# Optimization experiments

Measured on AMD Instinct MI355X. Metric: run time of the kernel, lower is better.

The kernel has to match this reference:

```python
import jax, jax.numpy as jnp
import numpy as np
import math

# Model dims (see shape_source)
BATCH, SEQ, HH, WW = 32, 128, 32, 32   # x: (B, seq_len, H, W); L = H*W = 1024
D_MODEL = 1024                          # hidden_dim
N2 = 4                                  # n=8 -> 4 complex S4D modes
L_MAX = 64                              # SSM kernel length (l_max)


def _layernorm(x, gamma, beta, eps=1e-5):
    mu = jnp.mean(x, axis=-1, keepdims=True)
    var = jnp.var(x, axis=-1, keepdims=True)
    return (x - mu) * jax.lax.rsqrt(var + eps) * gamma + beta


def setup_inputs() -> dict:
    key = jax.random.key(0)
    ks = jax.random.split(key, 12)
    d_in = SEQ  # d_input = d_output = seq_len
    inp = {
        "x": jax.random.normal(ks[0], (BATCH, SEQ, HH, WW), dtype=jnp.float32),
        # encoder Linear(d_input -> d_model)
        "W_enc": jax.random.normal(ks[1], (d_in, D_MODEL), dtype=jnp.float32) / math.sqrt(d_in),
        "b_enc": jnp.zeros((D_MODEL,), dtype=jnp.float32),
        # S4D SSM parameters (per d_model channel, N2 complex modes)
        "log_dt": (jax.random.uniform(ks[2], (D_MODEL,), dtype=jnp.float32)
                   * (math.log(0.1) - math.log(0.001)) + math.log(0.001)),
        "A_log_real": jnp.full((D_MODEL, N2), math.log(0.5), dtype=jnp.float32),
        "A_imag": jnp.broadcast_to(math.pi * jnp.arange(N2, dtype=jnp.float32), (D_MODEL, N2)).copy(),
        "C_real": jax.random.normal(ks[3], (D_MODEL, N2), dtype=jnp.float32) * 0.5,
        "C_imag": jax.random.normal(ks[4], (D_MODEL, N2), dtype=jnp.float32) * 0.5,
        "D": jax.random.normal(ks[5], (D_MODEL,), dtype=jnp.float32),
        # position-wise GLU mixing Linear(d_model -> 2*d_model)
        "W_glu": jax.random.normal(ks[6], (D_MODEL, 2 * D_MODEL), dtype=jnp.float32) / math.sqrt(D_MODEL),
        "b_glu": jnp.zeros((2 * D_MODEL,), dtype=jnp.float32),
        "ln_gamma": jnp.ones((D_MODEL,), dtype=jnp.float32),
        "ln_beta": jnp.zeros((D_MODEL,), dtype=jnp.float32),
        # decoder Linear(d_model -> d_output)
        "W_dec": jax.random.normal(ks[7], (D_MODEL, d_in), dtype=jnp.float32) / math.sqrt(D_MODEL),
        "b_dec": jnp.zeros((d_in,), dtype=jnp.float32),
    }
    return inp


def reference(x, W_enc, b_enc, log_dt, A_log_real, A_imag, C_real, C_imag, D,
              W_glu, b_glu, ln_gamma, ln_beta, W_dec, b_dec):
    Bsz, S, Hh, Ww = x.shape
    L = Hh * Ww
    u = x.reshape(Bsz, S, L)                                  # (B, d_input, L)
    # encoder applied per position along L
    h = jnp.einsum('bdl,de->ble', u, W_enc) + b_enc           # (B, L, d_model)

    # ---- S4D kernel (ZOH discretization, B=1, diagonal A) ----
    dt = jnp.exp(log_dt)                                      # (d,)
    A = -jnp.exp(A_log_real) + 1j * A_imag                    # (d, n2) complex
    Cc = C_real + 1j * C_imag
    dtA = A * dt[:, None]                                     # (d, n2)
    Bd = (jnp.exp(dtA) - 1.0) / A                             # ZOH input matrix
    t = jnp.arange(L_MAX)
    vand = jnp.exp(dtA[:, :, None] * t)                       # (d, n2, l_max)
    K = 2.0 * jnp.einsum('dn,dnl->dl', Cc * Bd, vand).real    # (d, l_max)

    # ---- causal FFT convolution along L + skip D*u ----
    z = jnp.swapaxes(h, 1, 2)                                 # (B, d, L)
    n_fft = L + L_MAX
    y = jnp.fft.irfft(jnp.fft.rfft(z, n=n_fft) * jnp.fft.rfft(K, n=n_fft), n=n_fft)[..., :L]
    y = y + D[:, None] * z                                    # (B, d, L)

    # ---- block: GELU -> GLU mixing -> residual -> LayerNorm ----
    y = jax.nn.gelu(jnp.swapaxes(y, 1, 2))                    # (B, L, d)
    g = y @ W_glu + b_glu                                     # (B, L, 2d)
    g = g[..., :D_MODEL] * jax.nn.sigmoid(g[..., D_MODEL:])
    h = _layernorm(h + g, ln_gamma, ln_beta)                  # (B, L, d)

    out = h @ W_dec + b_dec                                   # (B, L, d_output)
    out = jnp.swapaxes(out, 1, 2).reshape(Bsz, S, Hh, Ww)
    return out
```

## Files before the change

### kernel.cpp

```cpp
#include <hip/hip_runtime.h>
#include <hip/hip_bf16.h>
#include <math.h>

#define B_ 32
#define S_ 128
#define L_ 1024
#define D_ 1024

typedef unsigned short u16;
typedef __attribute__((ext_vector_type(8))) __bf16 bf16x8;
typedef __attribute__((ext_vector_type(8))) short short8;
typedef __attribute__((ext_vector_type(4))) float f32x4;

__device__ __forceinline__ float bf2f(u16 u) {
    return __uint_as_float(((unsigned)u) << 16);
}
__device__ __forceinline__ u16 f2bf(float f) {
    unsigned u = __float_as_uint(f);
    u += 0x7FFF + ((u >> 16) & 1);
    return (u16)(u >> 16);
}
__device__ __forceinline__ float gelu_tanh(float x) {
    float x3 = x * x * x;
    float t = tanhf(0.7978845608028654f * (x + 0.044715f * x3));
    return 0.5f * x * (1.0f + t);
}
__device__ __forceinline__ float sigmoidf(float x) {
    return 1.0f / (1.0f + expf(-x));
}
__device__ __forceinline__ void gld16(const void* g, void* l) {
    __builtin_amdgcn_global_load_lds((const __attribute__((address_space(1))) void*)g,
                                     (__attribute__((address_space(3))) void*)l, 16, 0, 0);
}

__device__ __forceinline__ void tcast_body(
        const float* __restrict__ src, u16* __restrict__ dst, int R, int C,
        const float* __restrict__ rowscale, int bx, int by, int t,
        float (*tile)[65]) {
    int c0 = bx * 64, r0 = by * 64;
    #pragma unroll
    for (int p = 0; p < 4; ++p) {
        int fid = p * 256 + t;
        int rr = fid >> 4, cc = (fid & 15) * 4;
        float4 v = *(const float4*)&src[(size_t)(r0 + rr) * C + c0 + cc];
        float sc = rowscale ? rowscale[r0 + rr] : 1.0f;
        tile[rr][cc + 0] = v.x * sc; tile[rr][cc + 1] = v.y * sc;
        tile[rr][cc + 2] = v.z * sc; tile[rr][cc + 3] = v.w * sc;
    }
    __syncthreads();
    #pragma unroll
    for (int p = 0; p < 4; ++p) {
        int fid = p * 256 + t;
        int rr = fid >> 4, cc = (fid & 15) * 4;
        ushort4 o;
        o.x = f2bf(tile[cc + 0][rr]);
        o.y = f2bf(tile[cc + 1][rr]);
        o.z = f2bf(tile[cc + 2][rr]);
        o.w = f2bf(tile[cc + 3][rr]);
        *(ushort4*)&dst[(size_t)(c0 + rr) * R + r0 + cc] = o;
    }
}

__global__ __launch_bounds__(256) void k_prep(
        const float* __restrict__ Wg, u16* __restrict__ WgT,
        const float* __restrict__ Wd, const float* __restrict__ gam,
        u16* __restrict__ WdT,
        const float* __restrict__ We, u16* __restrict__ WeT,
        const float* __restrict__ x, u16* __restrict__ xb,
        const float* __restrict__ ldt, const float* __restrict__ Alr,
        const float* __restrict__ Aim, const float* __restrict__ Cr,
        const float* __restrict__ Ci, float* __restrict__ Kt,
        const float* __restrict__ bet, const float* __restrict__ bd,
        float* __restrict__ c12) {
    __shared__ float tile[64][65];
    __shared__ float r1[4], r2[4];
    int blk = blockIdx.x;
    int t = threadIdx.x;
    if (blk < 512) {
        tcast_body(Wg, WgT, 1024, 2048, nullptr, blk & 31, blk >> 5, t, tile);
    } else if (blk < 544) {
        int id = blk - 512;
        tcast_body(Wd, WdT, 1024, 128, gam, id & 1, id >> 1, t, tile);
    } else if (blk < 576) {
        int id = blk - 544;
        tcast_body(We, WeT, 128, 1024, nullptr, id & 15, id >> 4, t, tile);
    } else if (blk < 1600) {
        int id = blk - 576;
        int bz = id >> 5;
        tcast_body(x + (size_t)bz * 131072, xb + (size_t)bz * 131072,
                   128, 1024, nullptr, id & 15, (id >> 4) & 1, t, tile);
    } else if (blk < 1856) {
        int tid = (blk - 1600) * 256 + t;
        int d = tid & (D_ - 1);
        int j = tid >> 10;
        float dt = expf(ldt[d]);
        float acc = 0.f;
        #pragma unroll
        for (int n = 0; n < 4; ++n) {
            float ar = -expf(Alr[d * 4 + n]);
            float ai = Aim[d * 4 + n];
            float wr = ar * dt, wi = ai * dt;
            float ew = expf(wr);
            float sw, cw; sincosf(wi, &sw, &cw);
            float ur = ew * cw - 1.0f, ui = ew * sw;
            float inv = 1.0f / (ar * ar + ai * ai);
            float bdr = (ur * ar + ui * ai) * inv;
            float bdi = (ui * ar - ur * ai) * inv;
            float cr = Cr[d * 4 + n], ci = Ci[d * 4 + n];
            float cbr = cr * bdr - ci * bdi;
            float cbi = cr * bdi + ci * bdr;
            float ej = expf(wr * (float)j);
            float sj, cj; sincosf(wi * (float)j, &sj, &cj);
            acc += 2.0f * ej * (cbr * cj - cbi * sj);
        }
        Kt[j * D_ + d] = acc;
    } else {
        int s = blk - 1856;
        float a1 = 0.f, a2 = 0.f;
        #pragma unroll
        for (int it = 0; it < 4; ++it) {
            int k = it * 256 + t;
            float w = Wd[(size_t)k * 128 + s];
            a1 += gam[k] * w;
            a2 += bet[k] * w;
        }
        #pragma unroll
        for (int off = 32; off > 0; off >>= 1) {
            a1 += __shfl_down(a1, off);
            a2 += __shfl_down(a2, off);
        }
        int wid = t >> 6, lane = t & 63;
        if (lane == 0) { r1[wid] = a1; r2[wid] = a2; }
        __syncthreads();
        if (t == 0) {
            c12[s] = r1[0] + r1[1] + r1[2] + r1[3];
            c12[128 + s] = r2[0] + r2[1] + r2[2] + r2[3] + bd[s];
        }
    }
}

__global__ __launch_bounds__(256, 4) void k_enc_mfma(
        const u16* __restrict__ xb, const u16* __restrict__ WeT,
        const float* __restrict__ be, u16* __restrict__ hb) {
    __shared__ __align__(16) u16 S[17408];
    u16* As = S;
    u16* Bs = S + 8192;
    int t = threadIdx.x;
    int lane = t & 63, wid = t >> 6;
    int wr = wid & 1, wc = wid >> 1;
    int orig = blockIdx.x;
    int wgid = (orig & 7) * 256 + (orig >> 3);
    int m0 = (wgid >> 3) * 128;
    int e0 = (wgid & 7) * 128;

    int gofs = (((lane & 7) ^ ((lane >> 3) & 7)) * 8);
    int rloc[4];
    #pragma unroll
    for (int c = 0; c < 4; ++c) rloc[c] = (wid * 4 + c) * 8 + (lane >> 3);
    int co[2];
    co[0] = (((lane >> 4) + 0) ^ (lane & 7)) * 8;
    co[1] = (((lane >> 4) + 4) ^ (lane & 7)) * 8;
    int arow[4], brow[4];
    #pragma unroll
    for (int i = 0; i < 4; ++i) arow[i] = (wr * 64 + i * 16 + (lane & 15)) * 64;
    #pragma unroll
    for (int q = 0; q < 4; ++q) brow[q] = (wc * 64 + q * 16 + (lane & 15)) * 64;

    f32x4 acc[4][4] = {};
    #pragma unroll
    for (int kt = 0; kt < 2; ++kt) {
        if (kt) __syncthreads();
        int k0 = kt * 64;
        #pragma unroll
        for (int c = 0; c < 4; ++c) {
            int ch = wid * 4 + c;
            gld16(&xb[(size_t)(m0 + rloc[c]) * 128 + k0 + gofs], &As[ch * 512]);
            gld16(&WeT[(size_t)(e0 + rloc[c]) * 128 + k0 + gofs], &Bs[ch * 512]);
        }
        __syncthreads();
        #pragma unroll
        for (int kh = 0; kh < 2; ++kh) {
            bf16x8 af[4], bfr[4];
            #pragma unroll
            for (int i = 0; i < 4; ++i) af[i] = *(const bf16x8*)&As[arow[i] + co[kh]];
            #pragma unroll
            for (int q = 0; q < 4; ++q) bfr[q] = *(const bf16x8*)&Bs[brow[q] + co[kh]];
            __builtin_amdgcn_s_setprio(1);
            #pragma unroll
            for (int i = 0; i < 4; ++i)
                #pragma unroll
                for (int q = 0; q < 4; ++q)
                    acc[i][q] = __builtin_amdgcn_mfma_f32_16x16x32_bf16(af[i], bfr[q], acc[i][q], 0, 0, 0);
            __builtin_amdgcn_s_setprio(0);
        }
    }
    __syncthreads();
    #pragma unroll
    for (int q = 0; q < 4; ++q) {
        int e = wc * 64 + q * 16 + (lane & 15);
        float bias = be[e0 + e];
        #pragma unroll
        for (int i = 0; i < 4; ++i)
            #pragma unroll
            for (int r = 0; r < 4; ++r) {
                int m = wr * 64 + i * 16 + (lane >> 4) * 4 + r;
                S[m * 136 + e] = f2bf(acc[i][q][r] + bias);
            }
    }
    __syncthreads();
    #pragma unroll
    for (int p = 0; p < 8; ++p) {
        int fid = p * 256 + t;
        int row = fid >> 4, cg = (fid & 15) * 8;
        *(uint4*)&hb[(size_t)(m0 + row) * 1024 + e0 + cg] = *(const uint4*)&S[row * 136 + cg];
    }
}

__global__ __launch_bounds__(256) void k_conv(
        const u16* __restrict__ hb, const float* __restrict__ Kt,
        const float* __restrict__ Dv, u16* __restrict__ yg) {
    __shared__ float hs[128][68];
    int b = blockIdx.y;
    int d0 = blockIdx.x * 64;
    int t = threadIdx.x;
    int dl = t & 63, lg = t >> 6;
    {
        int r = 64 + (t >> 2), cg0 = (t & 3) * 16;
        #pragma unroll
        for (int j = 0; j < 4; ++j)
            *(float4*)&hs[r][cg0 + j * 4] = make_float4(0.f, 0.f, 0.f, 0.f);
    }
    float kr[64];
    #pragma unroll
    for (int j = 0; j < 64; ++j) kr[j] = Kt[j * 1024 + d0 + dl];
    float Dd = Dv[d0 + dl];
    int lr = t >> 2, cg = (t & 3) * 16;
    uint4 pref0, pref1;
#define LOADP(IT) { const u16* src = &hb[((size_t)b * 1024 + (IT) * 64 + lr) * 1024 + d0 + cg]; \
    pref0 = *(const uint4*)&src[0]; pref1 = *(const uint4*)&src[8]; }
    LOADP(0);
    for (int it = 0; it < 16; ++it) {
        int l0 = it * 64;
        {
            int row = (l0 + lr) & 127;
            const u16* pu0 = (const u16*)&pref0;
            const u16* pu1 = (const u16*)&pref1;
            #pragma unroll
            for (int e = 0; e < 8; ++e) hs[row][cg + e] = bf2f(pu0[e]);
            #pragma unroll
            for (int e = 0; e < 8; ++e) hs[row][cg + 8 + e] = bf2f(pu1[e]);
        }
        __syncthreads();
        if (it < 15) LOADP(it + 1);
        float acc[16] = {};
        int rb = l0 + 65 + lg * 16;
        #pragma unroll
        for (int s = 0; s < 15; ++s) {
            float hv = hs[(rb + s) & 127][dl];
            #pragma unroll
            for (int i = 0; i <= 14; ++i)
                if (i <= s) acc[i] = fmaf(kr[i + 63 - s], hv, acc[i]);
        }
        #pragma unroll
        for (int s = 15; s < 64; ++s) {
            float hv = hs[(rb + s) & 127][dl];
            #pragma unroll
            for (int i = 0; i < 16; ++i)
                acc[i] = fmaf(kr[i + 63 - s], hv, acc[i]);
        }
        #pragma unroll
        for (int s = 64; s < 79; ++s) {
            float hv = hs[(rb + s) & 127][dl];
            #pragma unroll
            for (int i = 1; i < 16; ++i)
                if (i >= s - 63) acc[i] = fmaf(kr[i + 63 - s], hv, acc[i]);
        }
        #pragma unroll
        for (int i = 0; i < 16; ++i) {
            int l = l0 + lg * 16 + i;
            float z = hs[l & 127][dl];
            float y = acc[i] + Dd * z;
            yg[((size_t)b * 1024 + l) * 1024 + d0 + dl] = f2bf(gelu_tanh(y));
        }
        __syncthreads();
    }
#undef LOADP
}

__global__ __launch_bounds__(512, 2) void k_glu256(
        const u16* __restrict__ yg, const u16* __restrict__ WgT,
        const float* __restrict__ bg, u16* __restrict__ hb) {
    __shared__ u16 S[65536];
    int t = threadIdx.x;
    int lane = t & 63, wid = t >> 6;
    int wr = wid >> 2, wc = wid & 3;

    int orig = blockIdx.x;
    int wgid = (orig & 7) * 128 + (orig >> 3);
    int m0 = (wgid >> 3) * 256;
    int p0g = (wgid & 7) * 128;

    int gofs = (((lane & 7) ^ ((lane >> 3) & 7)) * 8);
    int ch0 = wid * 2, ch1 = ch0 + 1;
    int dst0 = ch0 * 512 + lane * 8;
    int dst1 = ch1 * 512 + lane * 8;
    int gmA[2][2], gmB[2][2];
    #pragma unroll
    for (int h = 0; h < 2; ++h) {
        #pragma unroll
        for (int j = 0; j < 2; ++j) {
            int ch = ch0 + j;
            gmA[h][j] = m0 + (ch >> 3) * 128 + h * 64 + (ch & 7) * 8 + (lane >> 3);
            int r = (ch >> 2) * 64 + h * 32 + (ch & 3) * 8 + (lane >> 3);
            gmB[h][j] = ((r >> 4) & 1) * 1024 + p0g + (((r >> 5) << 4) | (r & 15));
        }
    }
    int co[2];
    co[0] = (((lane >> 4) + 0) ^ (lane & 7)) * 8;
    co[1] = (((lane >> 4) + 4) ^ (lane & 7)) * 8;
    int arow[4], brow[2];
    #pragma unroll
    for (int i = 0; i < 4; ++i) arow[i] = (wr * 64 + i * 16 + (lane & 15)) * 64;
    #pragma unroll
    for (int q = 0; q < 2; ++q) brow[q] = (wc * 32 + q * 16 + (lane & 15)) * 64;

#define GLD_A(H, BUF, K0) { u16* d_ = &S[((BUF) * 2 + (H)) * 8192]; \
    gld16(&yg[(size_t)gmA[H][0] * 1024 + (K0) + gofs], d_ + dst0); \
    gld16(&yg[(size_t)gmA[H][1] * 1024 + (K0) + gofs], d_ + dst1); }
#define GLD_B(H, BUF, K0) { u16* d_ = &S[32768 + ((BUF) * 2 + (H)) * 8192]; \
    gld16(&WgT[(size_t)gmB[H][0] * 1024 + (K0) + gofs], d_ + dst0); \
    gld16(&WgT[(size_t)gmB[H][1] * 1024 + (K0) + gofs], d_ + dst1); }

#define RD_AH(MS) { const u16* Ar_ = &S[(cbuf * 2 + (MS)) * 8192]; \
    _Pragma("unroll") for (int i = 0; i < 4; ++i) { \
        a_[i][0] = *(const bf16x8*)&Ar_[arow[i] + co[0]]; \
        a_[i][1] = *(const bf16x8*)&Ar_[arow[i] + co[1]]; } }
#define RD_BH(NS, BB) { const u16* Br_ = &S[32768 + (cbuf * 2 + (NS)) * 8192]; \
    _Pragma("unroll") for (int q = 0; q < 2; ++q) { \
        BB[q][0] = *(const bf16x8*)&Br_[brow[q] + co[0]]; \
        BB[q][1] = *(const bf16x8*)&Br_[brow[q] + co[1]]; } }
#define MFMA16(MS, NS, BB) { __builtin_amdgcn_s_setprio(1); \
    _Pragma("unroll") for (int i = 0; i < 4; ++i) \
        _Pragma("unroll") for (int q = 0; q < 2; ++q) { \
            acc[(MS) * 4 + i][(NS) * 2 + q] = __builtin_amdgcn_mfma_f32_16x16x32_bf16( \
                a_[i][0], BB[q][0], acc[(MS) * 4 + i][(NS) * 2 + q], 0, 0, 0); \
            acc[(MS) * 4 + i][(NS) * 2 + q] = __builtin_amdgcn_mfma_f32_16x16x32_bf16( \
                a_[i][1], BB[q][1], acc[(MS) * 4 + i][(NS) * 2 + q], 0, 0, 0); } \
    __builtin_amdgcn_s_setprio(0); }

    f32x4 acc[8][4] = {};
    bf16x8 a_[4][2], b0_[2][2], b1_[2][2];

    GLD_A(0, 0, 0); GLD_B(0, 0, 0); GLD_B(1, 0, 0); GLD_A(1, 0, 0);
    GLD_A(0, 1, 64); GLD_B(0, 1, 64);

    for (int kt = 0; kt < 15; ++kt) {
        int cbuf = kt & 1, nbuf = cbuf ^ 1;
        int k1 = (kt + 1) * 64, k2 = (kt + 2) * 64;
        asm volatile("s_waitcnt vmcnt(4)" ::: "memory");
        __builtin_amdgcn_s_barrier();
        __builtin_amdgcn_sched_barrier(0);
        RD_AH(0); RD_BH(0, b0_); RD_BH(1, b1_);
        GLD_B(1, nbuf, k1);
        GLD_A(1, nbuf, k1);
        MFMA16(0, 0, b0_);
        MFMA16(0, 1, b1_);
        RD_AH(1);
        __builtin_amdgcn_s_barrier();
        __builtin_amdgcn_sched_barrier(0);
        if (kt < 14) { GLD_A(0, cbuf, k2); GLD_B(0, cbuf, k2); }
        MFMA16(1, 0, b0_);
        MFMA16(1, 1, b1_);
    }
    {
        int cbuf = 1;
        asm volatile("s_waitcnt vmcnt(0)" ::: "memory");
        __builtin_amdgcn_s_barrier();
        __builtin_amdgcn_sched_barrier(0);
        RD_AH(0); RD_BH(0, b0_); RD_BH(1, b1_);
        MFMA16(0, 0, b0_);
        MFMA16(0, 1, b1_);
        RD_AH(1);
        MFMA16(1, 0, b0_);
        MFMA16(1, 1, b1_);
    }
#undef GLD_A
#undef GLD_B
#undef RD_AH
#undef RD_BH
#undef MFMA16

    #pragma unroll
    for (int i = 0; i < 8; ++i) {
        #pragma unroll
        for (int pb = 0; pb < 2; ++pb) {
            int col = p0g + (wc * 2 + pb) * 16 + (lane & 15);
            float b1v = bg[col];
            float b2v = bg[1024 + col];
            #pragma unroll
            for (int r = 0; r < 4; ++r) {
                int m = m0 + wr * 128 + i * 16 + (lane >> 4) * 4 + r;
                size_t idx = (size_t)m * 1024 + col;
                float g1 = acc[i][pb * 2][r] + b1v;
                float g2 = acc[i][pb * 2 + 1][r] + b2v;
                hb[idx] = f2bf(bf2f(hb[idx]) + g1 * sigmoidf(g2));
            }
        }
    }
}

__global__ __launch_bounds__(256) void k_dec_mfma(
        const u16* __restrict__ hb, const u16* __restrict__ WdT,
        const float* __restrict__ c12, float* __restrict__ out) {
    __shared__ __align__(16) char smem[66560];
    u16* As = (u16*)smem;
    u16* Bs = (u16*)(smem + 32768);
    float* Ts = (float*)smem;
    float* muL = (float*)(smem + 65536);
    float* rsL = (float*)(smem + 65536 + 512);
    int t = threadIdx.x;
    int lane = t & 63, wid = t >> 6;
    int wr = wid & 1, wc = wid >> 1;
    int m0 = blockIdx.x * 128;
    int bb = m0 >> 10, l0 = m0 & 1023;

    int gsrc = (((lane & 7) ^ (lane >> 3)) * 8);
    int rr4[4];
    #pragma unroll
    for (int c = 0; c < 4; ++c) rr4[c] = (wid * 4 + c) * 8 + (lane >> 3);
    int co[2];
    co[0] = (((lane >> 4) + 0) ^ (lane & 7)) * 8;
    co[1] = (((lane >> 4) + 4) ^ (lane & 7)) * 8;
    int arow[4], brow[4];
    #pragma unroll
    for (int i = 0; i < 4; ++i) arow[i] = (wr * 64 + i * 16 + (lane & 15)) * 64;
    #pragma unroll
    for (int q = 0; q < 4; ++q) brow[q] = (wc * 64 + q * 16 + (lane & 15)) * 64;

    f32x4 acc[4][4] = {};
    float s1[4] = {}, s2[4] = {};
    #pragma unroll
    for (int c = 0; c < 4; ++c) {
        int ch = wid * 4 + c;
        gld16(&hb[(size_t)(m0 + rr4[c]) * 1024 + gsrc], &As[0 * 8192 + ch * 512]);
        gld16(&WdT[(size_t)rr4[c] * 1024 + gsrc], &Bs[0 * 8192 + ch * 512]);
    }
    __syncthreads();
    int cur = 0;
    for (int kt = 0; kt < 16; ++kt) {
        if (kt < 15) {
            int k0 = (kt + 1) * 64;
            #pragma unroll
            for (int c = 0; c < 4; ++c) {
                int ch = wid * 4 + c;
                gld16(&hb[(size_t)(m0 + rr4[c]) * 1024 + k0 + gsrc], &As[(cur ^ 1) * 8192 + ch * 512]);
                gld16(&WdT[(size_t)rr4[c] * 1024 + k0 + gsrc], &Bs[(cur ^ 1) * 8192 + ch * 512]);
            }
        }
        #pragma unroll
        for (int kh = 0; kh < 2; ++kh) {
            bf16x8 af[4], bfr[4];
            #pragma unroll
            for (int i = 0; i < 4; ++i) af[i] = *(const bf16x8*)&As[cur * 8192 + arow[i] + co[kh]];
            #pragma unroll
            for (int q = 0; q < 4; ++q) bfr[q] = *(const bf16x8*)&Bs[cur * 8192 + brow[q] + co[kh]];
            if (wid < 2) {
                #pragma unroll
                for (int i = 0; i < 4; ++i) {
                    short8 sa = *(short8*)&af[i];
                    #pragma unroll
                    for (int e = 0; e < 8; ++e) {
                        float v = bf2f((u16)sa[e]);
                        s1[i] += v;
                        s2[i] = fmaf(v, v, s2[i]);
                    }
                }
            }
            __builtin_amdgcn_s_setprio(1);
            #pragma unroll
            for (int i = 0; i < 4; ++i)
                #pragma unroll
                for (int q = 0; q < 4; ++q)
                    acc[i][q] = __builtin_amdgcn_mfma_f32_16x16x32_bf16(af[i], bfr[q], acc[i][q], 0, 0, 0);
            __builtin_amdgcn_s_setprio(0);
        }
        __syncthreads();
        cur ^= 1;
    }
    if (wid < 2) {
        #pragma unroll
        for (int i = 0; i < 4; ++i) {
            s1[i] += __shfl_xor(s1[i], 16);
            s2[i] += __shfl_xor(s2[i], 16);
            s1[i] += __shfl_xor(s1[i], 32);
            s2[i] += __shfl_xor(s2[i], 32);
            if (lane < 16) {
                int ml = wr * 64 + i * 16 + lane;
                float mu = s1[i] * (1.0f / 1024.0f);
                float var = s2[i] * (1.0f / 1024.0f) - mu * mu;
                muL[ml] = mu;
                rsL[ml] = rsqrtf(var + 1e-5f);
            }
        }
    }
    __syncthreads();
    #pragma unroll
    for (int ro = 0; ro < 2; ++ro) {
        if (wc == ro) {
            #pragma unroll
            for (int i = 0; i < 4; ++i)
                #pragma unroll
                for (int q = 0; q < 4; ++q) {
                    int sl = q * 16 + (lane & 15);
                    float c1v = c12[ro * 64 + sl];
                    float c2v = c12[128 + ro * 64 + sl];
                    #pragma unroll
                    for (int r = 0; r < 4; ++r) {
                        int ml = wr * 64 + i * 16 + (lane >> 4) * 4 + r;
                        float rst = rsL[ml];
                        Ts[sl * 132 + ml] = rst * acc[i][q][r] - muL[ml] * rst * c1v + c2v;
                    }
                }
        }
        __syncthreads();
        #pragma unroll
        for (int p = 0; p < 8; ++p) {
            int fid = p * 256 + t;
            int sl = fid >> 5, c = (fid & 31) * 4;
            float4 v = *(const float4*)&Ts[sl * 132 + c];
            *(float4*)&out[(size_t)bb * 131072 + (size_t)(ro * 64 + sl) * 1024 + l0 + c] = v;
        }
        __syncthreads();
    }
}

extern "C" void kernel_launch(void* const* d_in, const int* in_sizes, int n_in,
                              void* d_out, int out_size, void* d_ws, size_t ws_size,
                              hipStream_t stream) {
    (void)in_sizes; (void)n_in; (void)out_size; (void)ws_size;
    const float* x   = (const float*)d_in[0];
    const float* We  = (const float*)d_in[1];
    const float* be  = (const float*)d_in[2];
    const float* ldt = (const float*)d_in[3];
    const float* Alr = (const float*)d_in[4];
    const float* Aim = (const float*)d_in[5];
    const float* Cr  = (const float*)d_in[6];
    const float* Ci  = (const float*)d_in[7];
    const float* Dv  = (const float*)d_in[8];
    const float* Wg  = (const float*)d_in[9];
    const float* bg  = (const float*)d_in[10];
    const float* gam = (const float*)d_in[11];
    const float* bet = (const float*)d_in[12];
    const float* Wd  = (const float*)d_in[13];
    const float* bd  = (const float*)d_in[14];
    float* out = (float*)d_out;

    u16* hb = (u16*)d_ws;
    u16* yg = hb + 33554432ull;
    float* Kt = (float*)(yg + 33554432ull);
    u16* WgT = (u16*)(Kt + 65536);
    u16* WdT = WgT + 2097152ull;
    u16* WeT = WdT + 131072ull;
    float* c12 = (float*)(WeT + 131072ull);
    u16* xb  = yg;

    k_prep<<<1984, 256, 0, stream>>>(Wg, WgT, Wd, gam, WdT, We, WeT, x, xb,
                                     ldt, Alr, Aim, Cr, Ci, Kt, bet, bd, c12);
    k_enc_mfma<<<2048, 256, 0, stream>>>(xb, WeT, be, hb);
    k_conv<<<dim3(16, 32), 256, 0, stream>>>(hb, Kt, Dv, yg);
    k_glu256<<<1024, 512, 0, stream>>>(yg, WgT, bg, hb);
    k_dec_mfma<<<256, 256, 0, stream>>>(hb, WdT, c12, out);
}
```

Before: 323.9 us.

## Load GLU weight fragments directly from global into registers, skipping LDS staging

The B operand (GLU weights) of the GLU GEMM is now read straight from global memory into per-wave register fragments, with double buffering in even and odd register sets, instead of being staged through shared memory. Only the A tiles still go through LDS, which halves the LDS footprint and removes the B-side LDS reads. The cost is more VGPRs for the prefetched B fragments, a different vmcnt accounting, and uncoalesced 16-byte global reads of the weights that rely on L2 reuse across workgroups.

```diff
diff --git a/kernel.cpp b/kernel.cpp
--- a/kernel.cpp
+++ b/kernel.cpp
@@ -290,7 +290,7 @@
 __global__ __launch_bounds__(512, 2) void k_glu256(
         const u16* __restrict__ yg, const u16* __restrict__ WgT,
         const float* __restrict__ bg, u16* __restrict__ hb) {
-    __shared__ u16 S[65536];
+    __shared__ u16 S[32768];
     int t = threadIdx.x;
     int lane = t & 63, wid = t >> 6;
     int wr = wid >> 2, wc = wid & 3;
@@ -304,91 +304,87 @@
     int ch0 = wid * 2, ch1 = ch0 + 1;
     int dst0 = ch0 * 512 + lane * 8;
     int dst1 = ch1 * 512 + lane * 8;
-    int gmA[2][2], gmB[2][2];
+    int gmA[2][2];
     #pragma unroll
     for (int h = 0; h < 2; ++h) {
         #pragma unroll
         for (int j = 0; j < 2; ++j) {
             int ch = ch0 + j;
             gmA[h][j] = m0 + (ch >> 3) * 128 + h * 64 + (ch & 7) * 8 + (lane >> 3);
-            int r = (ch >> 2) * 64 + h * 32 + (ch & 3) * 8 + (lane >> 3);
-            gmB[h][j] = ((r >> 4) & 1) * 1024 + p0g + (((r >> 5) << 4) | (r & 15));
         }
     }
     int co[2];
     co[0] = (((lane >> 4) + 0) ^ (lane & 7)) * 8;
     co[1] = (((lane >> 4) + 4) ^ (lane & 7)) * 8;
-    int arow[4], brow[2];
+    int arow[4];
     #pragma unroll
     for (int i = 0; i < 4; ++i) arow[i] = (wr * 64 + i * 16 + (lane & 15)) * 64;
-    #pragma unroll
-    for (int q = 0; q < 2; ++q) brow[q] = (wc * 32 + q * 16 + (lane & 15)) * 64;
+    int grB[2][2];
+    #pragma unroll
+    for (int h = 0; h < 2; ++h)
+        #pragma unroll
+        for (int q = 0; q < 2; ++q) {
+            int tr = wc * 64 + h * 32 + q * 16 + (lane & 15);
+            grB[h][q] = ((tr >> 4) & 1) * 1024 + p0g + ((tr >> 5) << 4) + (tr & 15);
+        }
+    int kb[2];
+    kb[0] = (lane >> 4) * 8;
+    kb[1] = ((lane >> 4) + 4) * 8;
 
 #define GLD_A(H, BUF, K0) { u16* d_ = &S[((BUF) * 2 + (H)) * 8192]; \
     gld16(&yg[(size_t)gmA[H][0] * 1024 + (K0) + gofs], d_ + dst0); \
     gld16(&yg[(size_t)gmA[H][1] * 1024 + (K0) + gofs], d_ + dst1); }
-#define GLD_B(H, BUF, K0) { u16* d_ = &S[32768 + ((BUF) * 2 + (H)) * 8192]; \
-    gld16(&WgT[(size_t)gmB[H][0] * 1024 + (K0) + gofs], d_ + dst0); \
-    gld16(&WgT[(size_t)gmB[H][1] * 1024 + (K0) + gofs], d_ + dst1); }
-
-#define RD_AH(MS) { const u16* Ar_ = &S[(cbuf * 2 + (MS)) * 8192]; \
+#define LD_B(BB, K0) { _Pragma("unroll") for (int h = 0; h < 2; ++h) \
+    _Pragma("unroll") for (int q = 0; q < 2; ++q) \
+        _Pragma("unroll") for (int kh = 0; kh < 2; ++kh) \
+            BB[h][q][kh] = *(const bf16x8*)&WgT[(size_t)grB[h][q] * 1024 + (K0) + kb[kh]]; }
+#define RD_AH(MS, CB) { const u16* Ar_ = &S[((CB) * 2 + (MS)) * 8192]; \
     _Pragma("unroll") for (int i = 0; i < 4; ++i) { \
         a_[i][0] = *(const bf16x8*)&Ar_[arow[i] + co[0]]; \
         a_[i][1] = *(const bf16x8*)&Ar_[arow[i] + co[1]]; } }
-#define RD_BH(NS, BB) { const u16* Br_ = &S[32768 + (cbuf * 2 + (NS)) * 8192]; \
-    _Pragma("unroll") for (int q = 0; q < 2; ++q) { \
-        BB[q][0] = *(const bf16x8*)&Br_[brow[q] + co[0]]; \
-        BB[q][1] = *(const bf16x8*)&Br_[brow[q] + co[1]]; } }
 #define MFMA16(MS, NS, BB) { __builtin_amdgcn_s_setprio(1); \
     _Pragma("unroll") for (int i = 0; i < 4; ++i) \
         _Pragma("unroll") for (int q = 0; q < 2; ++q) { \
             acc[(MS) * 4 + i][(NS) * 2 + q] = __builtin_amdgcn_mfma_f32_16x16x32_bf16( \
-                a_[i][0], BB[q][0], acc[(MS) * 4 + i][(NS) * 2 + q], 0, 0, 0); \
+                a_[i][0], BB[(NS)][q][0], acc[(MS) * 4 + i][(NS) * 2 + q], 0, 0, 0); \
             acc[(MS) * 4 + i][(NS) * 2 + q] = __builtin_amdgcn_mfma_f32_16x16x32_bf16( \
-                a_[i][1], BB[q][1], acc[(MS) * 4 + i][(NS) * 2 + q], 0, 0, 0); } \
+                a_[i][1], BB[(NS)][q][1], acc[(MS) * 4 + i][(NS) * 2 + q], 0, 0, 0); } \
     __builtin_amdgcn_s_setprio(0); }
+#define TILE(KT, BB, WAITN, DO_STAGE) { \
+    asm volatile("s_waitcnt vmcnt(" #WAITN ")" ::: "memory"); \
+    __builtin_amdgcn_s_barrier(); \
+    __builtin_amdgcn_sched_barrier(0); \
+    int cb_ = (KT) & 1; \
+    RD_AH(0, cb_); \
+    MFMA16(0, 0, BB); \
+    MFMA16(0, 1, BB); \
+    RD_AH(1, cb_); \
+    __builtin_amdgcn_s_barrier(); \
+    __builtin_amdgcn_sched_barrier(0); \
+    if (DO_STAGE) { GLD_A(0, cb_, ((KT) + 2) * 64); GLD_A(1, cb_, ((KT) + 2) * 64); } \
+    MFMA16(1, 0, BB); \
+    MFMA16(1, 1, BB); \
+    if (DO_STAGE) LD_B(BB, ((KT) + 2) * 64); }
 
     f32x4 acc[8][4] = {};
-    bf16x8 a_[4][2], b0_[2][2], b1_[2][2];
-
-    GLD_A(0, 0, 0); GLD_B(0, 0, 0); GLD_B(1, 0, 0); GLD_A(1, 0, 0);
-    GLD_A(0, 1, 64); GLD_B(0, 1, 64);
-
-    for (int kt = 0; kt < 15; ++kt) {
-        int cbuf = kt & 1, nbuf = cbuf ^ 1;
-        int k1 = (kt + 1) * 64, k2 = (kt + 2) * 64;
-        asm volatile("s_waitcnt vmcnt(4)" ::: "memory");
-        __builtin_amdgcn_s_barrier();
-        __builtin_amdgcn_sched_barrier(0);
-        RD_AH(0); RD_BH(0, b0_); RD_BH(1, b1_);
-        GLD_B(1, nbuf, k1);
-        GLD_A(1, nbuf, k1);
-        MFMA16(0, 0, b0_);
-        MFMA16(0, 1, b1_);
-        RD_AH(1);
-        __builtin_amdgcn_s_barrier();
-        __builtin_amdgcn_sched_barrier(0);
-        if (kt < 14) { GLD_A(0, cbuf, k2); GLD_B(0, cbuf, k2); }
-        MFMA16(1, 0, b0_);
-        MFMA16(1, 1, b1_);
-    }
-    {
-        int cbuf = 1;
-        asm volatile("s_waitcnt vmcnt(0)" ::: "memory");
-        __builtin_amdgcn_s_barrier();
-        __builtin_amdgcn_sched_barrier(0);
-        RD_AH(0); RD_BH(0, b0_); RD_BH(1, b1_);
-        MFMA16(0, 0, b0_);
-        MFMA16(0, 1, b1_);
-        RD_AH(1);
-        MFMA16(1, 0, b0_);
-        MFMA16(1, 1, b1_);
-    }
+    bf16x8 a_[4][2], bE[2][2][2], bO[2][2][2];
+
+    LD_B(bE, 0);
+    GLD_A(0, 0, 0); GLD_A(1, 0, 0);
+    LD_B(bO, 64);
+    GLD_A(0, 1, 64); GLD_A(1, 1, 64);
+
+    for (int kt = 0; kt < 14; kt += 2) {
+        TILE(kt, bE, 12, 1);
+        TILE(kt + 1, bO, 12, 1);
+    }
+    TILE(14, bE, 12, 0);
+    TILE(15, bO, 0, 0);
 #undef GLD_A
-#undef GLD_B
+#undef LD_B
 #undef RD_AH
-#undef RD_BH
 #undef MFMA16
+#undef TILE
 
     #pragma unroll
     for (int i = 0; i < 8; ++i) {
```

Measured after the change: 382.5 us. 1.18x slower.
